# Kernel tuning notes

Hardware: AMD Instinct MI355X
Metric: run time of the kernel (lower is better)

The kernel has to match this reference:

```python
import jax, jax.numpy as jnp
import numpy as np

D_MODEL = 512
H = 8


def setup_inputs() -> dict:
    key = jax.random.key(0)
    ks = jax.random.split(key, 11)
    B, L, D = 8, 1024, D_MODEL
    s = 1.0 / np.sqrt(D)
    return {
        "q": jax.random.normal(ks[0], (B, L, D), jnp.float32),
        "k": jax.random.normal(ks[1], (B, L, D), jnp.float32),
        "v": jax.random.normal(ks[2], (B, L, D), jnp.float32),
        "Wq": jax.random.normal(ks[3], (D, D), jnp.float32) * s,
        "bq": jnp.zeros((D,), jnp.float32),
        "Wk": jax.random.normal(ks[4], (D, D), jnp.float32) * s,
        "bk": jnp.zeros((D,), jnp.float32),
        "Wv": jax.random.normal(ks[5], (D, D), jnp.float32) * s,
        "bv": jnp.zeros((D,), jnp.float32),
        "Wo": jax.random.normal(ks[6], (D, D), jnp.float32) * s,
        "bo": jnp.zeros((D,), jnp.float32),
    }


def _split_heads(x, h):
    B, L, D = x.shape
    return x.reshape(B, L, h, D // h).transpose(0, 2, 1, 3)  # (B,h,L,dk)


def reference(q, k, v, Wq, bq, Wk, bk, Wv, bv, Wo, bo):
    B, L, D = q.shape
    dk = D // H
    qw = q @ Wq + bq
    kw = k @ Wk + bk
    vw = q @ Wv + bv  # faithful to source bug: dense_v applied to q, not v
    qh = _split_heads(qw, H)
    kh = _split_heads(kw, H)
    vh = _split_heads(vw, H)
    scale = jnp.asarray(1.0 / np.sqrt(dk), qh.dtype)
    scores = jnp.einsum("bhqd,bhkd->bhqk", qh, kh) * scale  # (B,h,L,L)
    attn = jax.nn.softmax(scores, axis=-1)
    ctx = jnp.einsum("bhqk,bhkd->bhqd", attn, vh)  # (B,h,L,dk)
    out = ctx.transpose(0, 2, 1, 3).reshape(B, L, D) @ Wo + bo
    return out, attn
```

## Files before the change

### kernel.cpp

```cpp
#include <hip/hip_runtime.h>

typedef unsigned short u16;
typedef __bf16 bf16x8 __attribute__((ext_vector_type(8)));
typedef unsigned short u16x8 __attribute__((ext_vector_type(8)));
typedef unsigned short u16x4 __attribute__((ext_vector_type(4)));
typedef float f32x4 __attribute__((ext_vector_type(4)));

#define MFMA16(a, b, c) __builtin_amdgcn_mfma_f32_16x16x32_bf16(a, b, c, 0, 0, 0)

__device__ __forceinline__ u16 f2bf(float f) {
    union { float f; unsigned u; } v; v.f = f;
    unsigned r = v.u + 0x7fffu + ((v.u >> 16) & 1u);
    return (u16)(r >> 16);
}
__device__ __forceinline__ float bf2f(u16 u) {
    union { unsigned u; float f; } v; v.u = (unsigned)u << 16;
    return v.f;
}
__device__ __forceinline__ u16 bfc(float f) {
    return __builtin_bit_cast(u16, (__bf16)f);
}

typedef __attribute__((address_space(1))) void GAS;
typedef __attribute__((address_space(3))) void LAS;
__device__ __forceinline__ void gload_lds16(const void* g, void* l) {
    __builtin_amdgcn_global_load_lds((GAS*)g, (LAS*)l, 16, 0, 0);
}

__global__ __launch_bounds__(256) void wtrans(const float* Wq, const float* Wk,
                                              const float* Wv, const float* Wo, u16* WT) {
    __shared__ float t[32][33];
    const int z = blockIdx.z;
    const float* W = (z == 0) ? Wq : (z == 1) ? Wk : (z == 2) ? Wv : Wo;
    u16* out = WT + (size_t)z * 512 * 512;
    const int tx = threadIdx.x, ty = threadIdx.y;
    const int k0 = blockIdx.y * 32, n0 = blockIdx.x * 32;
#pragma unroll
    for (int p = 0; p < 4; ++p)
        t[ty + 8 * p][tx] = W[(size_t)(k0 + ty + 8 * p) * 512 + n0 + tx];
    __syncthreads();
#pragma unroll
    for (int p = 0; p < 4; ++p) {
        const int n = n0 + ty + 8 * p;
        out[(size_t)n * 512 + k0 + tx] = f2bf(t[tx][ty + 8 * p]);
    }
}

__global__ __launch_bounds__(256) void qkconv(const float* q, const float* k, u16* qb, u16* kb) {
    const size_t n4 = (size_t)8192 * 512 / 4;
    const size_t stride = (size_t)gridDim.x * 256;
    for (size_t i = (size_t)blockIdx.x * 256 + threadIdx.x; i < 2 * n4; i += stride) {
        const float4 v = (i < n4) ? ((const float4*)q)[i] : ((const float4*)k)[i - n4];
        u16x4 o;
        o[0] = f2bf(v.x); o[1] = f2bf(v.y); o[2] = f2bf(v.z); o[3] = f2bf(v.w);
        if (i < n4) ((u16x4*)qb)[i] = o; else ((u16x4*)kb)[i - n4] = o;
    }
}

template <int CMODE>
__device__ __forceinline__ void gemm_core(const u16* A, const u16* Bt,
                                          const float* bias, void* Cp,
                                          int bm, int bn) {
    __shared__ u16 As[128 * 64];
    __shared__ u16 Bs[128 * 64];
    const int tid  = threadIdx.x;
    const int lane = tid & 63;
    const int w    = tid >> 6;
    const int wm   = (w >> 1) * 64;
    const int wn   = (w & 1) * 64;
    const int col  = lane & 15;
    const int quad = lane >> 4;
    const int srow = lane >> 3;
    const int scol = (lane & 7) * 8;

    f32x4 acc[4][4] = {};

    for (int kt = 0; kt < 512; kt += 64) {
        __syncthreads();
#pragma unroll
        for (int p = 0; p < 4; ++p) {
            const int c  = w * 4 + p;
            const int gr = c * 8 + srow;
            gload_lds16(A  + (size_t)(bm * 128 + gr) * 512 + kt + scol, As + c * 512);
            gload_lds16(Bt + (size_t)(bn * 128 + gr) * 512 + kt + scol, Bs + c * 512);
        }
        __syncthreads();
#pragma unroll
        for (int ks = 0; ks < 2; ++ks) {
            const int k0 = ks * 32 + quad * 8;
            bf16x8 af[4], bfr[4];
#pragma unroll
            for (int i = 0; i < 4; ++i)
                af[i] = __builtin_bit_cast(bf16x8, *(const u16x8*)(As + (wm + i * 16 + col) * 64 + k0));
#pragma unroll
            for (int j = 0; j < 4; ++j)
                bfr[j] = __builtin_bit_cast(bf16x8, *(const u16x8*)(Bs + (wn + j * 16 + col) * 64 + k0));
#pragma unroll
            for (int i = 0; i < 4; ++i)
#pragma unroll
                for (int j = 0; j < 4; ++j)
                    acc[i][j] = MFMA16(af[i], bfr[j], acc[i][j]);
        }
    }
#pragma unroll
    for (int j = 0; j < 4; ++j) {
        const int gn = bn * 128 + wn + j * 16 + col;
        const float bv = bias[gn];
#pragma unroll
        for (int i = 0; i < 4; ++i) {
            if (CMODE == 2) {
                const int gm0 = bm * 128 + wm + i * 16 + quad * 4;
                u16x4 pk;
#pragma unroll
                for (int r = 0; r < 4; ++r) pk[r] = f2bf(acc[i][j][r] + bv);
                u16* dst = (u16*)Cp
                    + ((size_t)((gm0 >> 10) * 8 + (gn >> 6)) * 64 + (gn & 63)) * 1024
                    + (gm0 & 1023);
                *(u16x4*)dst = pk;
            } else {
#pragma unroll
                for (int r = 0; r < 4; ++r) {
                    const int gm = bm * 128 + wm + i * 16 + quad * 4 + r;
                    const float val = acc[i][j][r] + bv;
                    if (CMODE == 1) ((float*)Cp)[(size_t)gm * 512 + gn] = val;
                    else            ((u16*)Cp)[(size_t)gm * 512 + gn]   = f2bf(val);
                }
            }
        }
    }
}

__global__ __launch_bounds__(256, 3) void qkv_gemm(const u16* qb, const u16* kb, const u16* WT,
                                                   const float* bq, const float* bk, const float* bv,
                                                   u16* qkw, u16* vt) {
    const int z = blockIdx.z;
    const u16* B = WT + (size_t)z * 512 * 512;
    if (z == 0)
        gemm_core<0>(qb, B, bq, qkw, blockIdx.x, blockIdx.y);
    else if (z == 1)
        gemm_core<0>(kb, B, bk, qkw + (size_t)8192 * 512, blockIdx.x, blockIdx.y);
    else
        gemm_core<2>(qb, B, bv, vt, blockIdx.x, blockIdx.y);
}

__global__ __launch_bounds__(256, 3) void out_gemm(const u16* ctx, const u16* WoT,
                                                   const float* bo, float* out) {
    gemm_core<1>(ctx, WoT, bo, out, blockIdx.x, blockIdx.y);
}

__global__ __launch_bounds__(512, 4) void attn_kernel(const u16* qw, const u16* kw, const u16* vt,
                                                      float* attn_out, u16* ctx) {
    __shared__ u16 Ks[128 * 72];
    __shared__ u16 Vs[64 * 136];
    __shared__ u16 Ps[8][16 * 136];

    const int bh  = blockIdx.x;
    const int qt  = blockIdx.y;
    const int b   = bh >> 3, h = bh & 7;
    const int tid = threadIdx.x;
    const int lane = tid & 63, w = tid >> 6;
    const int col = lane & 15, quad = lane >> 4;
    const int wq  = w * 16;
    const float scale = 0.125f;

    const size_t headbase = (size_t)b * (1024 * 512) + (size_t)h * 64;
    const u16* vh = vt + (size_t)bh * (64 * 1024);

    const int krow = tid >> 2, koff = (tid & 3) * 16;
    const int vrow = tid >> 3, voff = (tid & 7) * 16;
    const u16* kbase = kw + headbase + (size_t)krow * 512 + koff;
    const u16* vbase = vh + (size_t)vrow * 1024 + voff;

    float* arow = attn_out + ((size_t)bh * 1024 + (size_t)(qt * 128 + wq + col)) * 1024;

    bf16x8 qf[2];
    {
        const u16* qp = qw + headbase + (size_t)(qt * 128 + wq + col) * 512 + quad * 8;
        qf[0] = __builtin_bit_cast(bf16x8, *(const u16x8*)qp);
        qf[1] = __builtin_bit_cast(bf16x8, *(const u16x8*)(qp + 32));
    }

    float l_acc = 0.f;

    u16x8 rk0 = *(const u16x8*)kbase;
    u16x8 rk1 = *(const u16x8*)(kbase + 8);
    for (int kt = 0; kt < 8; ++kt) {
        __syncthreads();
        *(u16x8*)(Ks + krow * 72 + koff)     = rk0;
        *(u16x8*)(Ks + krow * 72 + koff + 8) = rk1;
        __syncthreads();
        if (kt < 7) {
            const u16* kp = kbase + (size_t)(kt + 1) * (128 * 512);
            rk0 = *(const u16x8*)kp;
            rk1 = *(const u16x8*)(kp + 8);
        }
        f32x4 s[8] = {};
#pragma unroll
        for (int ks = 0; ks < 2; ++ks) {
            const int k0 = ks * 32 + quad * 8;
#pragma unroll
            for (int j = 0; j < 8; ++j) {
                const bf16x8 kf = __builtin_bit_cast(bf16x8,
                    *(const u16x8*)(Ks + (j * 16 + col) * 72 + k0));
                s[j] = MFMA16(kf, qf[ks], s[j]);
            }
        }
#pragma unroll
        for (int j = 0; j < 8; ++j)
#pragma unroll
            for (int r = 0; r < 4; ++r)
                l_acc += __expf(s[j][r] * scale);
    }

    float rinv;
    {
        float l = l_acc;
        l += __shfl_xor(l, 16); l += __shfl_xor(l, 32);
        rinv = 1.0f / l;
    }

    f32x4 o[4] = {};

    rk0 = *(const u16x8*)kbase;
    rk1 = *(const u16x8*)(kbase + 8);
    u16x8 rv0 = *(const u16x8*)vbase;
    u16x8 rv1 = *(const u16x8*)(vbase + 8);
    for (int kt = 0; kt < 8; ++kt) {
        __syncthreads();
        *(u16x8*)(Ks + krow * 72 + koff)      = rk0;
        *(u16x8*)(Ks + krow * 72 + koff + 8)  = rk1;
        *(u16x8*)(Vs + vrow * 136 + voff)     = rv0;
        *(u16x8*)(Vs + vrow * 136 + voff + 8) = rv1;
        __syncthreads();
        if (kt < 7) {
            const u16* kp = kbase + (size_t)(kt + 1) * (128 * 512);
            rk0 = *(const u16x8*)kp;
            rk1 = *(const u16x8*)(kp + 8);
            const u16* vp = vbase + (kt + 1) * 128;
            rv0 = *(const u16x8*)vp;
            rv1 = *(const u16x8*)(vp + 8);
        }
        u16* pw = &Ps[w][0];
        float* atile = arow + kt * 128;
#pragma unroll
        for (int half = 0; half < 2; ++half) {
            f32x4 s[4] = {};
#pragma unroll
            for (int ks = 0; ks < 2; ++ks) {
                const int k0 = ks * 32 + quad * 8;
#pragma unroll
                for (int j = 0; j < 4; ++j) {
                    const bf16x8 kf = __builtin_bit_cast(bf16x8,
                        *(const u16x8*)(Ks + (half * 64 + j * 16 + col) * 72 + k0));
                    s[j] = MFMA16(kf, qf[ks], s[j]);
                }
            }
#pragma unroll
            for (int j = 0; j < 4; ++j) {
                f32x4 pn;
#pragma unroll
                for (int r = 0; r < 4; ++r)
                    pn[r] = __expf(s[j][r] * scale) * rinv;
                *(f32x4*)(atile + half * 64 + j * 16 + quad * 4) = pn;
                u16x4 pk;
                pk[0] = bfc(pn[0]); pk[1] = bfc(pn[1]);
                pk[2] = bfc(pn[2]); pk[3] = bfc(pn[3]);
                *(u16x4*)(pw + col * 136 + half * 64 + j * 16 + quad * 4) = pk;
            }
        }
#pragma unroll
        for (int ks = 0; ks < 4; ++ks) {
            const int k0 = ks * 32 + quad * 8;
            const bf16x8 pf = __builtin_bit_cast(bf16x8, *(const u16x8*)(pw + col * 136 + k0));
#pragma unroll
            for (int j = 0; j < 4; ++j) {
                const bf16x8 vf = __builtin_bit_cast(bf16x8,
                    *(const u16x8*)(Vs + (j * 16 + col) * 136 + k0));
                o[j] = MFMA16(pf, vf, o[j]);
            }
        }
    }

#pragma unroll
    for (int j = 0; j < 4; ++j)
#pragma unroll
        for (int r = 0; r < 4; ++r) {
            const int qg = qt * 128 + wq + quad * 4 + r;
            ctx[(size_t)(b * 1024 + qg) * 512 + h * 64 + j * 16 + col] = f2bf(o[j][r]);
        }
}

extern "C" void kernel_launch(void* const* d_in, const int* in_sizes, int n_in,
                              void* d_out, int out_size, void* d_ws, size_t ws_size,
                              hipStream_t stream) {
    (void)in_sizes; (void)n_in; (void)out_size; (void)ws_size;
    const float* q  = (const float*)d_in[0];
    const float* k  = (const float*)d_in[1];
    const float* Wq = (const float*)d_in[3];
    const float* bq = (const float*)d_in[4];
    const float* Wk = (const float*)d_in[5];
    const float* bk = (const float*)d_in[6];
    const float* Wv = (const float*)d_in[7];
    const float* bv = (const float*)d_in[8];
    const float* Wo = (const float*)d_in[9];
    const float* bo = (const float*)d_in[10];

    float* out  = (float*)d_out;
    float* attn = (float*)d_out + (size_t)8 * 1024 * 512;

    char* ws = (char*)d_ws;
    u16* WT  = (u16*)ws;
    u16* qb  = (u16*)(ws + (size_t)2 * 1024 * 1024);
    u16* kb  = qb + (size_t)8192 * 512;
    u16* qkv = kb + (size_t)8192 * 512;
    u16* qw  = qkv;
    u16* kw  = qkv + (size_t)8192 * 512;
    u16* vt  = qkv + (size_t)2 * 8192 * 512;
    u16* ctx = qkv + (size_t)3 * 8192 * 512;

    wtrans     <<<dim3(16, 16, 4), dim3(32, 8), 0, stream>>>(Wq, Wk, Wv, Wo, WT);
    qkconv     <<<dim3(2048),      256,          0, stream>>>(q, k, qb, kb);
    qkv_gemm   <<<dim3(64, 4, 3),  256,          0, stream>>>(qb, kb, WT, bq, bk, bv, qkv, vt);
    attn_kernel<<<dim3(64, 8),     512,          0, stream>>>(qw, kw, vt, attn, ctx);
    out_gemm   <<<dim3(64, 4),     256,          0, stream>>>(ctx, WT + (size_t)3 * 512 * 512, bo, out);
}
```

Measured before the change: 412.8 us.

## Fuse softmax into one pass with deferred normalization and register-held probabilities

Replaces the two-pass attention (one pass to sum the exponentials, one to recompute scores) with a single pass. Each exponential is summed as it is produced, and P·V is accumulated on the unnormalized probabilities. The row sum is applied to ctx at the end. The bf16-packed exponentials are kept in a 64-entry register array so the fp32 attention matrix can be normalized and written after the loop. This removes the second QK^T computation and the K reload. In exchange, the returned attention values are rebuilt from bf16-rounded exponentials, and the large register array plus the lowered occupancy hint may cause spills or reduce latency hiding. Deferring all attention stores to the end also removes their overlap with compute.

```diff
diff --git a/kernel.cpp b/kernel.cpp
--- a/kernel.cpp
+++ b/kernel.cpp
@@ -148,7 +148,7 @@
     gemm_core<1>(ctx, WoT, bo, out, blockIdx.x, blockIdx.y);
 }
 
-__global__ __launch_bounds__(512, 4) void attn_kernel(const u16* qw, const u16* kw, const u16* vt,
+__global__ __launch_bounds__(512, 2) void attn_kernel(const u16* qw, const u16* kw, const u16* vt,
                                                       float* attn_out, u16* ctx) {
     __shared__ u16 Ks[128 * 72];
     __shared__ u16 Vs[64 * 136];
@@ -181,50 +181,14 @@
     }
 
     float l_acc = 0.f;
+    f32x4 o[4] = {};
+    u16x4 preg[8][8];
 
     u16x8 rk0 = *(const u16x8*)kbase;
     u16x8 rk1 = *(const u16x8*)(kbase + 8);
-    for (int kt = 0; kt < 8; ++kt) {
-        __syncthreads();
-        *(u16x8*)(Ks + krow * 72 + koff)     = rk0;
-        *(u16x8*)(Ks + krow * 72 + koff + 8) = rk1;
-        __syncthreads();
-        if (kt < 7) {
-            const u16* kp = kbase + (size_t)(kt + 1) * (128 * 512);
-            rk0 = *(const u16x8*)kp;
-            rk1 = *(const u16x8*)(kp + 8);
-        }
-        f32x4 s[8] = {};
-#pragma unroll
-        for (int ks = 0; ks < 2; ++ks) {
-            const int k0 = ks * 32 + quad * 8;
-#pragma unroll
-            for (int j = 0; j < 8; ++j) {
-                const bf16x8 kf = __builtin_bit_cast(bf16x8,
-                    *(const u16x8*)(Ks + (j * 16 + col) * 72 + k0));
-                s[j] = MFMA16(kf, qf[ks], s[j]);
-            }
-        }
-#pragma unroll
-        for (int j = 0; j < 8; ++j)
-#pragma unroll
-            for (int r = 0; r < 4; ++r)
-                l_acc += __expf(s[j][r] * scale);
-    }
-
-    float rinv;
-    {
-        float l = l_acc;
-        l += __shfl_xor(l, 16); l += __shfl_xor(l, 32);
-        rinv = 1.0f / l;
-    }
-
-    f32x4 o[4] = {};
-
-    rk0 = *(const u16x8*)kbase;
-    rk1 = *(const u16x8*)(kbase + 8);
     u16x8 rv0 = *(const u16x8*)vbase;
     u16x8 rv1 = *(const u16x8*)(vbase + 8);
+#pragma unroll
     for (int kt = 0; kt < 8; ++kt) {
         __syncthreads();
         *(u16x8*)(Ks + krow * 72 + koff)      = rk0;
@@ -241,7 +205,6 @@
             rv1 = *(const u16x8*)(vp + 8);
         }
         u16* pw = &Ps[w][0];
-        float* atile = arow + kt * 128;
 #pragma unroll
         for (int half = 0; half < 2; ++half) {
             f32x4 s[4] = {};
@@ -257,14 +220,15 @@
             }
 #pragma unroll
             for (int j = 0; j < 4; ++j) {
-                f32x4 pn;
+                f32x4 e;
 #pragma unroll
                 for (int r = 0; r < 4; ++r)
-                    pn[r] = __expf(s[j][r] * scale) * rinv;
-                *(f32x4*)(atile + half * 64 + j * 16 + quad * 4) = pn;
+                    e[r] = __expf(s[j][r] * scale);
+                l_acc += (e[0] + e[1]) + (e[2] + e[3]);
                 u16x4 pk;
-                pk[0] = bfc(pn[0]); pk[1] = bfc(pn[1]);
-                pk[2] = bfc(pn[2]); pk[3] = bfc(pn[3]);
+                pk[0] = bfc(e[0]); pk[1] = bfc(e[1]);
+                pk[2] = bfc(e[2]); pk[3] = bfc(e[3]);
+                preg[kt][half * 4 + j] = pk;
                 *(u16x4*)(pw + col * 136 + half * 64 + j * 16 + quad * 4) = pk;
             }
         }
@@ -281,12 +245,34 @@
         }
     }
 
+    float rinv;
+    {
+        float l = l_acc;
+        l += __shfl_xor(l, 16); l += __shfl_xor(l, 32);
+        rinv = 1.0f / l;
+    }
+    float ri[4];
+#pragma unroll
+    for (int r = 0; r < 4; ++r)
+        ri[r] = __shfl(rinv, quad * 4 + r);
+
 #pragma unroll
     for (int j = 0; j < 4; ++j)
 #pragma unroll
         for (int r = 0; r < 4; ++r) {
             const int qg = qt * 128 + wq + quad * 4 + r;
-            ctx[(size_t)(b * 1024 + qg) * 512 + h * 64 + j * 16 + col] = f2bf(o[j][r]);
+            ctx[(size_t)(b * 1024 + qg) * 512 + h * 64 + j * 16 + col] = f2bf(o[j][r] * ri[r]);
+        }
+
+#pragma unroll
+    for (int kt = 0; kt < 8; ++kt)
+#pragma unroll
+        for (int hj = 0; hj < 8; ++hj) {
+            const u16x4 pk = preg[kt][hj];
+            f32x4 pn;
+            pn[0] = bf2f(pk[0]) * rinv; pn[1] = bf2f(pk[1]) * rinv;
+            pn[2] = bf2f(pk[2]) * rinv; pn[3] = bf2f(pk[3]) * rinv;
+            *(f32x4*)(arow + kt * 128 + (hj >> 2) * 64 + (hj & 3) * 16 + quad * 4) = pn;
         }
 }
 
```

Measured after the change: 421.5 us. +2.1%, slower.
